# Optimization experiments

Measured on AMD Instinct MI355X. Metric: run time of the kernel, lower is better.

## Reference

```python
import jax, jax.numpy as jnp
import numpy as np

LN_EPS = 1e-12
NEG_INF = -1e9


def setup_inputs() -> dict:
    key = jax.random.key(0)
    ks = jax.random.split(key, 4)
    B, S, H = 8, 2048, 1024
    inputs = jax.random.normal(ks[0], (B, S, H), dtype=jnp.float32)
    masks = jnp.ones((B, S), dtype=jnp.int32)
    scale = 1.0 / np.sqrt(H)
    Wq = jax.random.normal(ks[1], (H, H), dtype=jnp.float32) * scale
    bq = jnp.zeros((H,), dtype=jnp.float32)
    Wk = jax.random.normal(ks[2], (H, H), dtype=jnp.float32) * scale
    bk = jnp.zeros((H,), dtype=jnp.float32)
    ln_gamma = jnp.ones((H,), dtype=jnp.float32)
    ln_beta = jnp.zeros((H,), dtype=jnp.float32)
    return {"inputs": inputs, "masks": masks, "Wq": Wq, "bq": bq,
            "Wk": Wk, "bk": bk, "ln_gamma": ln_gamma, "ln_beta": ln_beta}


def _layernorm(x, gamma, beta):
    mu = jnp.mean(x, axis=-1, keepdims=True)
    var = jnp.mean(jnp.square(x - mu), axis=-1, keepdims=True)
    return (x - mu) * jax.lax.rsqrt(var + LN_EPS) * gamma + beta


def reference(inputs, masks, Wq, bq, Wk, bk, ln_gamma, ln_beta):
    # inputs: [B,S,H]; masks: [B,S] (1 = keep key position)
    H = inputs.shape[-1]
    query = inputs @ Wq + bq                      # [B,S,H]
    key_ = inputs @ Wk + bk                       # [B,S,H]
    scores = jnp.einsum('bqh,bkh->bqk', query, key_) * (1.0 / jnp.sqrt(jnp.float32(H)))
    # logits_mask: invalid key positions get large negative logit
    scores = jnp.where(masks[:, None, :] != 0, scores, NEG_INF)
    probs = jax.nn.softmax(scores, axis=-1)       # [B,S,S]
    context = jnp.einsum('bqk,bkh->bqh', probs, inputs)  # value = raw inputs
    return _layernorm(inputs + context, ln_gamma, ln_beta)
```

## Files before the change

### kernel.cpp

```cpp
#include <hip/hip_runtime.h>
#include <stdint.h>
#include <stddef.h>

typedef _Float16 f16_t;
typedef _Float16 f16x8 __attribute__((ext_vector_type(8)));
typedef _Float16 f16x4 __attribute__((ext_vector_type(4)));
typedef float    f32x4 __attribute__((ext_vector_type(4)));

#define AS_G __attribute__((address_space(1)))
#define AS_L __attribute__((address_space(3)))

__device__ __forceinline__ void gload_lds16(const void* g, void* l) {
  __builtin_amdgcn_global_load_lds((const AS_G uint32_t*)g, (AS_L uint32_t*)l, 16, 0, 0);
}

#define LN_EPS 1e-12f

__global__ __launch_bounds__(256) void cast_f16_kernel(const float* __restrict__ in,
                                                       f16_t* __restrict__ out) {
  int i = blockIdx.x * 256 + threadIdx.x;
  float4 v = ((const float4*)in)[i];
  f16x4 o = {(f16_t)v.x, (f16_t)v.y, (f16_t)v.z, (f16_t)v.w};
  ((f16x4*)out)[i] = o;
}

__global__ __launch_bounds__(256) void transpose_f16_kernel(const float* __restrict__ in,
                                                            f16_t* __restrict__ out,
                                                            int R, int C) {
  __shared__ float tile[32][33];
  int b = blockIdx.z;
  const float* inb = in + (size_t)b * R * C;
  f16_t* outb = out + (size_t)b * R * C;
  int tx = threadIdx.x, ty = threadIdx.y;
  int c0 = blockIdx.x * 32, r0 = blockIdx.y * 32;
#pragma unroll
  for (int i = 0; i < 32; i += 8)
    tile[ty + i][tx] = inb[(size_t)(r0 + ty + i) * C + (c0 + tx)];
  __syncthreads();
#pragma unroll
  for (int i = 0; i < 32; i += 8)
    outb[(size_t)(c0 + ty + i) * R + (r0 + tx)] = (f16_t)tile[tx][ty + i];
}

__global__ __launch_bounds__(256) void wvec_kernel(const float* __restrict__ Wq,
                                                   const float* __restrict__ bq,
                                                   const float* __restrict__ Wk,
                                                   const float* __restrict__ bk,
                                                   float* __restrict__ wqbk,
                                                   float* __restrict__ wkbq,
                                                   float* __restrict__ c0) {
  __shared__ float red[4];
  int bid = blockIdx.x, tid = threadIdx.x;
  const float* rowp; const float* vecp; float* outp;
  if (bid < 1024)      { rowp = Wq + (size_t)bid * 1024; vecp = bk; outp = wqbk + bid; }
  else if (bid < 2048) { rowp = Wk + (size_t)(bid - 1024) * 1024; vecp = bq; outp = wkbq + (bid - 1024); }
  else                 { rowp = bq; vecp = bk; outp = c0; }
  float4 a = ((const float4*)rowp)[tid];
  float4 b = ((const float4*)vecp)[tid];
  float s = a.x * b.x + a.y * b.y + a.z * b.z + a.w * b.w;
#pragma unroll
  for (int off = 32; off > 0; off >>= 1) s += __shfl_xor(s, off, 64);
  if ((tid & 63) == 0) red[tid >> 6] = s;
  __syncthreads();
  if (tid == 0) *outp = red[0] + red[1] + red[2] + red[3];
}

__global__ __launch_bounds__(256) void cqck_kernel(const float* __restrict__ X,
                                                   const float* __restrict__ wqbk,
                                                   const float* __restrict__ wkbq,
                                                   float* __restrict__ cq,
                                                   float* __restrict__ ck) {
  __shared__ float r1[4], r2[4];
  int m = blockIdx.x, tid = threadIdx.x;
  float4 x = ((const float4*)(X + (size_t)m * 1024))[tid];
  float4 a = ((const float4*)wqbk)[tid];
  float4 b = ((const float4*)wkbq)[tid];
  float s1 = x.x * a.x + x.y * a.y + x.z * a.z + x.w * a.w;
  float s2 = x.x * b.x + x.y * b.y + x.z * b.z + x.w * b.w;
#pragma unroll
  for (int off = 32; off > 0; off >>= 1) { s1 += __shfl_xor(s1, off, 64); s2 += __shfl_xor(s2, off, 64); }
  if ((tid & 63) == 0) { r1[tid >> 6] = s1; r2[tid >> 6] = s2; }
  __syncthreads();
  if (tid == 0) {
    cq[m] = r1[0] + r1[1] + r1[2] + r1[3];
    ck[m] = r2[0] + r2[1] + r2[2] + r2[3];
  }
}

__global__ __launch_bounds__(256) void gemm_bt_kernel(
    const f16_t* __restrict__ A, const f16_t* __restrict__ Bt, f16_t* __restrict__ C,
    const float* __restrict__ cq, const float* __restrict__ ck, const float* __restrict__ c0p,
    const int* __restrict__ mask, const float* __restrict__ invl, float* __restrict__ lpart,
    int lda, int ldb, int ldc, int K, float scale, int mode,
    size_t sA, size_t sB, size_t sC) {
  __shared__ f16_t As[2][128 * 32];
  __shared__ f16_t Bs[2][128 * 32];

  const int tid = threadIdx.x;
  const int lane = tid & 63;
  const int wv = tid >> 6;
  const int m16 = lane & 15;
  const int quad = lane >> 4;
  const int wr = (wv >> 1) * 64;
  const int wc = (wv & 1) * 64;

  const f16_t* Ab = A + blockIdx.z * sA + (size_t)blockIdx.x * 128 * lda;
  const f16_t* Bb = Bt + blockIdx.z * sB + (size_t)blockIdx.y * 128 * ldb;

  const int ch = ((lane & 3) ^ ((lane >> 3) & 3)) * 8;
  const int r0 = wv * 32 + (lane >> 2);
  const f16_t* gA0 = Ab + (size_t)r0 * lda + ch;
  const f16_t* gA1 = Ab + (size_t)(r0 + 16) * lda + ch;
  const f16_t* gB0 = Bb + (size_t)r0 * ldb + ch;
  const f16_t* gB1 = Bb + (size_t)(r0 + 16) * ldb + ch;
  const int ldsA0 = (wv * 32) * 32, ldsA1 = (wv * 32 + 16) * 32;

  const int aslot = (quad ^ ((m16 >> 1) & 3)) * 8;
  int aoff[4], boff[4];
#pragma unroll
  for (int t = 0; t < 4; ++t) {
    aoff[t] = (wr + t * 16 + m16) * 32 + aslot;
    boff[t] = (wc + t * 16 + m16) * 32 + aslot;
  }

  f32x4 acc[4][4] = {};
  const int nk = K >> 5;

  gload_lds16(gA0, &As[0][ldsA0]);
  gload_lds16(gA1, &As[0][ldsA1]);
  gload_lds16(gB0, &Bs[0][ldsA0]);
  gload_lds16(gB1, &Bs[0][ldsA1]);

  int buf = 0;
  for (int it = 0; it < nk; ++it) {
    if (it + 1 < nk) {
      const int k0 = (it + 1) << 5;
      gload_lds16(gA0 + k0, &As[buf ^ 1][ldsA0]);
      gload_lds16(gA1 + k0, &As[buf ^ 1][ldsA1]);
      gload_lds16(gB0 + k0, &Bs[buf ^ 1][ldsA0]);
      gload_lds16(gB1 + k0, &Bs[buf ^ 1][ldsA1]);
      asm volatile("s_waitcnt vmcnt(4)" ::: "memory");
    } else {
      asm volatile("s_waitcnt vmcnt(0)" ::: "memory");
    }
    asm volatile("s_barrier" ::: "memory");

    f16x8 af[4], bfr[4];
#pragma unroll
    for (int t = 0; t < 4; ++t) {
      af[t]  = *(const f16x8*)&As[buf][aoff[t]];
      bfr[t] = *(const f16x8*)&Bs[buf][boff[t]];
    }
#pragma unroll
    for (int rt = 0; rt < 4; ++rt)
#pragma unroll
      for (int ct = 0; ct < 4; ++ct)
        acc[rt][ct] = __builtin_amdgcn_mfma_f32_16x16x32_f16(af[rt], bfr[ct], acc[rt][ct], 0, 0, 0);

    asm volatile("s_barrier" ::: "memory");
    buf ^= 1;
  }

  f16_t* Cb = C + blockIdx.z * sC;
  const int row0 = blockIdx.x * 128 + wr + quad * 4;
  const int col0 = blockIdx.y * 128 + wc + m16;
  if (mode == 0) {
#pragma unroll
    for (int ct = 0; ct < 4; ++ct)
#pragma unroll
      for (int rt = 0; rt < 4; ++rt)
#pragma unroll
        for (int r = 0; r < 4; ++r)
          Cb[(size_t)(row0 + rt * 16 + r) * ldc + col0 + ct * 16] = (f16_t)acc[rt][ct][r];
  } else if (mode == 1) {
    const int* mp = mask + blockIdx.z * 2048;
    const size_t rowg0 = blockIdx.z * 2048 + row0;
    const float c0 = *c0p;
    float rsum[4][4];
#pragma unroll
    for (int rt = 0; rt < 4; ++rt)
#pragma unroll
      for (int r = 0; r < 4; ++r) rsum[rt][r] = 0.f;
#pragma unroll
    for (int ct = 0; ct < 4; ++ct) {
      int col = col0 + ct * 16;
      bool keep = (mp[col] != 0);
      float ckv = ck[blockIdx.z * 2048 + col];
#pragma unroll
      for (int rt = 0; rt < 4; ++rt)
#pragma unroll
        for (int r = 0; r < 4; ++r) {
          float cqv = cq[rowg0 + rt * 16 + r];
          float p = keep ? __expf((acc[rt][ct][r] + cqv + ckv + c0) * scale) : 0.f;
          rsum[rt][r] += p;
          Cb[(size_t)(row0 + rt * 16 + r) * ldc + col] = (f16_t)p;
        }
    }
    const int chunk = blockIdx.y * 2 + (wv & 1);
#pragma unroll
    for (int rt = 0; rt < 4; ++rt)
#pragma unroll
      for (int r = 0; r < 4; ++r) {
        float v = rsum[rt][r];
        v += __shfl_xor(v, 1, 16);
        v += __shfl_xor(v, 2, 16);
        v += __shfl_xor(v, 4, 16);
        v += __shfl_xor(v, 8, 16);
        if (m16 == 0) lpart[(rowg0 + rt * 16 + r) * 32 + chunk] = v;
      }
  } else {
    const size_t rowg0 = blockIdx.z * 2048 + row0;
#pragma unroll
    for (int rt = 0; rt < 4; ++rt)
#pragma unroll
      for (int r = 0; r < 4; ++r) {
        float il = invl[rowg0 + rt * 16 + r];
#pragma unroll
        for (int ct = 0; ct < 4; ++ct)
          Cb[(size_t)(row0 + rt * 16 + r) * ldc + col0 + ct * 16] = (f16_t)(acc[rt][ct][r] * il);
      }
  }
}

__global__ __launch_bounds__(256) void lreduce_kernel(const float* __restrict__ lpart,
                                                      float* __restrict__ invl) {
  int m = blockIdx.x * 256 + threadIdx.x;
  const float4* p = (const float4*)(lpart + (size_t)m * 32);
  float s = 0.f;
#pragma unroll
  for (int j = 0; j < 8; ++j) {
    float4 v = p[j];
    s += v.x + v.y + v.z + v.w;
  }
  invl[m] = 1.0f / fmaxf(s, 1e-30f);
}

__global__ __launch_bounds__(256) void ln_kernel(const float* __restrict__ X,
                                                 const f16_t* __restrict__ Ctx,
                                                 const float* __restrict__ gamma,
                                                 const float* __restrict__ beta,
                                                 float* __restrict__ out) {
  __shared__ float r1[4], r2[4];
  const int tid = threadIdx.x;
  const size_t base = (size_t)blockIdx.x * 1024;
  float4 xv = ((const float4*)(X + base))[tid];
  f16x4 cv = ((const f16x4*)(Ctx + base))[tid];
  float v0 = xv.x + (float)cv[0];
  float v1 = xv.y + (float)cv[1];
  float v2 = xv.z + (float)cv[2];
  float v3 = xv.w + (float)cv[3];
  float s1 = v0 + v1 + v2 + v3;
  float s2 = v0 * v0 + v1 * v1 + v2 * v2 + v3 * v3;
#pragma unroll
  for (int off = 32; off > 0; off >>= 1) {
    s1 += __shfl_xor(s1, off, 64);
    s2 += __shfl_xor(s2, off, 64);
  }
  if ((tid & 63) == 0) { r1[tid >> 6] = s1; r2[tid >> 6] = s2; }
  __syncthreads();
  s1 = r1[0] + r1[1] + r1[2] + r1[3];
  s2 = r2[0] + r2[1] + r2[2] + r2[3];
  float mu = s1 * (1.0f / 1024.0f);
  float var = s2 * (1.0f / 1024.0f) - mu * mu;
  float rs = rsqrtf(fmaxf(var, 0.0f) + LN_EPS);
  float4 gv = ((const float4*)gamma)[tid];
  float4 bv = ((const float4*)beta)[tid];
  float4 o;
  o.x = (v0 - mu) * rs * gv.x + bv.x;
  o.y = (v1 - mu) * rs * gv.y + bv.y;
  o.z = (v2 - mu) * rs * gv.z + bv.z;
  o.w = (v3 - mu) * rs * gv.w + bv.w;
  ((float4*)(out + base))[tid] = o;
}

extern "C" void kernel_launch(void* const* d_in, const int* in_sizes, int n_in,
                              void* d_out, int out_size, void* d_ws, size_t ws_size,
                              hipStream_t stream) {
  const float* X     = (const float*)d_in[0];
  const int*   masks = (const int*)d_in[1];
  const float* Wq    = (const float*)d_in[2];
  const float* bq    = (const float*)d_in[3];
  const float* Wk    = (const float*)d_in[4];
  const float* bk    = (const float*)d_in[5];
  const float* gamma = (const float*)d_in[6];
  const float* beta  = (const float*)d_in[7];
  float* out = (float*)d_out;

  if (ws_size < 115343360u) return;
  char* ws = (char*)d_ws;
  f16_t* Xb   = (f16_t*)(ws + 0);
  f16_t* Xt   = (f16_t*)(ws + 33554432);
  f16_t* T    = (f16_t*)(ws + 67108864);
  f16_t* Wqf  = (f16_t*)(ws + 100663296);
  f16_t* Wkf  = (f16_t*)(ws + 102760448);
  f16_t* Wkq  = (f16_t*)(ws + 104857600);
  float* lpart= (float*)(ws + 106954752);
  float* cq   = (float*)(ws + 109051904);
  float* ck   = (float*)(ws + 109117440);
  float* invl = (float*)(ws + 109182976);
  float* wqbk = (float*)(ws + 109248512);
  float* wkbq = (float*)(ws + 109252608);
  float* c0   = (float*)(ws + 109256704);
  f16_t* Ctx  = Xb;
  f16_t* probs = (f16_t*)d_out;

  const size_t SH = 2048u * 1024u;
  const size_t SS = 2048u * 2048u;
  const size_t HS = 1024u * 2048u;

  cast_f16_kernel<<<16384, 256, 0, stream>>>(X, Xb);
  cast_f16_kernel<<<1024, 256, 0, stream>>>(Wq, Wqf);
  cast_f16_kernel<<<1024, 256, 0, stream>>>(Wk, Wkf);
  transpose_f16_kernel<<<dim3(32, 64, 8), dim3(32, 8), 0, stream>>>(X, Xt, 2048, 1024);
  wvec_kernel<<<2049, 256, 0, stream>>>(Wq, bq, Wk, bk, wqbk, wkbq, c0);
  cqck_kernel<<<16384, 256, 0, stream>>>(X, wqbk, wkbq, cq, ck);

  gemm_bt_kernel<<<dim3(8, 8, 1), 256, 0, stream>>>(
      Wkf, Wqf, Wkq, nullptr, nullptr, nullptr, nullptr, nullptr, nullptr,
      1024, 1024, 1024, 1024, 0.f, 0, 0, 0, 0);

  gemm_bt_kernel<<<dim3(128, 8, 1), 256, 0, stream>>>(
      Xb, Wkq, T, nullptr, nullptr, nullptr, nullptr, nullptr, nullptr,
      1024, 1024, 1024, 1024, 0.f, 0, 0, 0, 0);

  gemm_bt_kernel<<<dim3(16, 16, 8), 256, 0, stream>>>(
      T, Xb, probs, cq, ck, c0, masks, nullptr, lpart,
      1024, 1024, 2048, 1024, 0.03125f, 1, SH, SH, SS);

  lreduce_kernel<<<64, 256, 0, stream>>>(lpart, invl);

  gemm_bt_kernel<<<dim3(16, 8, 8), 256, 0, stream>>>(
      probs, Xt, Ctx, nullptr, nullptr, nullptr, nullptr, invl, nullptr,
      2048, 2048, 1024, 2048, 0.f, 2, SS, HS, SH);

  ln_kernel<<<16384, 256, 0, stream>>>(X, Ctx, gamma, beta, out);
}
```

Baseline: 504.4 us.

## Fuse X cast with transpose and switch GEMM to single-buffered BK=64 tiles

Merges the f32->f16 cast of X into the transpose kernel so X is read once and both the row-major and transposed f16 copies come from the same load. The GEMM main loop drops the double-buffered 32-wide K pipeline for a single-buffered 64-wide K tile with a new XOR swizzle and two MFMA sub-steps per tile. Each tile now waits with __syncthreads before compute and again after it. This halves the barrier count per K but gives up the overlap of global loads with MFMA work, so load latency is exposed each iteration.

```diff
diff --git a/kernel.cpp b/kernel.cpp
--- a/kernel.cpp
+++ b/kernel.cpp
@@ -24,22 +24,26 @@
   ((f16x4*)out)[i] = o;
 }
 
-__global__ __launch_bounds__(256) void transpose_f16_kernel(const float* __restrict__ in,
-                                                            f16_t* __restrict__ out,
-                                                            int R, int C) {
+__global__ __launch_bounds__(256) void xprep_kernel(const float* __restrict__ in,
+                                                    f16_t* __restrict__ xb,
+                                                    f16_t* __restrict__ xt) {
   __shared__ float tile[32][33];
   int b = blockIdx.z;
-  const float* inb = in + (size_t)b * R * C;
-  f16_t* outb = out + (size_t)b * R * C;
+  const float* inb = in + (size_t)b * 2048 * 1024;
+  f16_t* xbb = xb + (size_t)b * 2048 * 1024;
+  f16_t* xtb = xt + (size_t)b * 1024 * 2048;
   int tx = threadIdx.x, ty = threadIdx.y;
   int c0 = blockIdx.x * 32, r0 = blockIdx.y * 32;
 #pragma unroll
+  for (int i = 0; i < 32; i += 8) {
+    float v = inb[(size_t)(r0 + ty + i) * 1024 + (c0 + tx)];
+    tile[ty + i][tx] = v;
+    xbb[(size_t)(r0 + ty + i) * 1024 + (c0 + tx)] = (f16_t)v;
+  }
+  __syncthreads();
+#pragma unroll
   for (int i = 0; i < 32; i += 8)
-    tile[ty + i][tx] = inb[(size_t)(r0 + ty + i) * C + (c0 + tx)];
-  __syncthreads();
-#pragma unroll
-  for (int i = 0; i < 32; i += 8)
-    outb[(size_t)(c0 + ty + i) * R + (r0 + tx)] = (f16_t)tile[tx][ty + i];
+    xtb[(size_t)(c0 + ty + i) * 2048 + (r0 + tx)] = (f16_t)tile[tx][ty + i];
 }
 
 __global__ __launch_bounds__(256) void wvec_kernel(const float* __restrict__ Wq,
@@ -93,8 +97,8 @@
     const int* __restrict__ mask, const float* __restrict__ invl, float* __restrict__ lpart,
     int lda, int ldb, int ldc, int K, float scale, int mode,
     size_t sA, size_t sB, size_t sC) {
-  __shared__ f16_t As[2][128 * 32];
-  __shared__ f16_t Bs[2][128 * 32];
+  __shared__ f16_t As[128 * 64];
+  __shared__ f16_t Bs[128 * 64];
 
   const int tid = threadIdx.x;
   const int lane = tid & 63;
@@ -107,58 +111,54 @@
   const f16_t* Ab = A + blockIdx.z * sA + (size_t)blockIdx.x * 128 * lda;
   const f16_t* Bb = Bt + blockIdx.z * sB + (size_t)blockIdx.y * 128 * ldb;
 
-  const int ch = ((lane & 3) ^ ((lane >> 3) & 3)) * 8;
-  const int r0 = wv * 32 + (lane >> 2);
-  const f16_t* gA0 = Ab + (size_t)r0 * lda + ch;
-  const f16_t* gA1 = Ab + (size_t)(r0 + 16) * lda + ch;
-  const f16_t* gB0 = Bb + (size_t)r0 * ldb + ch;
-  const f16_t* gB1 = Bb + (size_t)(r0 + 16) * ldb + ch;
-  const int ldsA0 = (wv * 32) * 32, ldsA1 = (wv * 32 + 16) * 32;
-
-  const int aslot = (quad ^ ((m16 >> 1) & 3)) * 8;
-  int aoff[4], boff[4];
+  const int lr8 = lane >> 3;
+  const int ch8 = (lane & 7) ^ lr8;
+  const f16_t* gA[4]; const f16_t* gB[4];
+  f16_t* lA[4]; f16_t* lB[4];
+#pragma unroll
+  for (int j = 0; j < 4; ++j) {
+    int row = wv * 32 + j * 8 + lr8;
+    gA[j] = Ab + (size_t)row * lda + ch8 * 8;
+    gB[j] = Bb + (size_t)row * ldb + ch8 * 8;
+    lA[j] = &As[(wv * 32 + j * 8) * 64];
+    lB[j] = &Bs[(wv * 32 + j * 8) * 64];
+  }
+
+  int aoff[4], boff[4], swz[2];
 #pragma unroll
   for (int t = 0; t < 4; ++t) {
-    aoff[t] = (wr + t * 16 + m16) * 32 + aslot;
-    boff[t] = (wc + t * 16 + m16) * 32 + aslot;
-  }
+    aoff[t] = (wr + t * 16 + m16) * 64;
+    boff[t] = (wc + t * 16 + m16) * 64;
+  }
+#pragma unroll
+  for (int s = 0; s < 2; ++s)
+    swz[s] = (((s << 2) | quad) ^ (m16 & 7)) * 8;
 
   f32x4 acc[4][4] = {};
-  const int nk = K >> 5;
-
-  gload_lds16(gA0, &As[0][ldsA0]);
-  gload_lds16(gA1, &As[0][ldsA1]);
-  gload_lds16(gB0, &Bs[0][ldsA0]);
-  gload_lds16(gB1, &Bs[0][ldsA1]);
-
-  int buf = 0;
-  for (int it = 0; it < nk; ++it) {
-    if (it + 1 < nk) {
-      const int k0 = (it + 1) << 5;
-      gload_lds16(gA0 + k0, &As[buf ^ 1][ldsA0]);
-      gload_lds16(gA1 + k0, &As[buf ^ 1][ldsA1]);
-      gload_lds16(gB0 + k0, &Bs[buf ^ 1][ldsA0]);
-      gload_lds16(gB1 + k0, &Bs[buf ^ 1][ldsA1]);
-      asm volatile("s_waitcnt vmcnt(4)" ::: "memory");
-    } else {
-      asm volatile("s_waitcnt vmcnt(0)" ::: "memory");
+
+  for (int k0 = 0; k0 < K; k0 += 64) {
+#pragma unroll
+    for (int j = 0; j < 4; ++j) {
+      gload_lds16(gA[j] + k0, lA[j]);
+      gload_lds16(gB[j] + k0, lB[j]);
     }
-    asm volatile("s_barrier" ::: "memory");
-
-    f16x8 af[4], bfr[4];
-#pragma unroll
-    for (int t = 0; t < 4; ++t) {
-      af[t]  = *(const f16x8*)&As[buf][aoff[t]];
-      bfr[t] = *(const f16x8*)&Bs[buf][boff[t]];
+    __syncthreads();
+
+#pragma unroll
+    for (int s = 0; s < 2; ++s) {
+      f16x8 af[4], bfr[4];
+#pragma unroll
+      for (int t = 0; t < 4; ++t) {
+        af[t]  = *(const f16x8*)&As[aoff[t] + swz[s]];
+        bfr[t] = *(const f16x8*)&Bs[boff[t] + swz[s]];
+      }
+#pragma unroll
+      for (int rt = 0; rt < 4; ++rt)
+#pragma unroll
+        for (int ct = 0; ct < 4; ++ct)
+          acc[rt][ct] = __builtin_amdgcn_mfma_f32_16x16x32_f16(af[rt], bfr[ct], acc[rt][ct], 0, 0, 0);
     }
-#pragma unroll
-    for (int rt = 0; rt < 4; ++rt)
-#pragma unroll
-      for (int ct = 0; ct < 4; ++ct)
-        acc[rt][ct] = __builtin_amdgcn_mfma_f32_16x16x32_f16(af[rt], bfr[ct], acc[rt][ct], 0, 0, 0);
-
-    asm volatile("s_barrier" ::: "memory");
-    buf ^= 1;
+    __syncthreads();
   }
 
   f16_t* Cb = C + blockIdx.z * sC;
@@ -308,10 +308,9 @@
   const size_t SS = 2048u * 2048u;
   const size_t HS = 1024u * 2048u;
 
-  cast_f16_kernel<<<16384, 256, 0, stream>>>(X, Xb);
+  xprep_kernel<<<dim3(32, 64, 8), dim3(32, 8), 0, stream>>>(X, Xb, Xt);
   cast_f16_kernel<<<1024, 256, 0, stream>>>(Wq, Wqf);
   cast_f16_kernel<<<1024, 256, 0, stream>>>(Wk, Wkf);
-  transpose_f16_kernel<<<dim3(32, 64, 8), dim3(32, 8), 0, stream>>>(X, Xt, 2048, 1024);
   wvec_kernel<<<2049, 256, 0, stream>>>(Wq, bq, Wk, bk, wqbk, wkbq, c0);
   cqck_kernel<<<16384, 256, 0, stream>>>(X, wqbk, wkbq, cq, ck);
 
```

New measurement: 479.2 us. 1.05x faster.
